# Kernel optimization log

Measured on AMD Instinct MI355X. Metric: run time of the kernel, lower is better.

Reference implementation:

```python
import jax, jax.numpy as jnp
import numpy as np

NS = 0.4      # neighborhood_size
GS = 8        # grid_size
RNN = 128     # rnn_size
EMB = 64      # embedding_size
NMIX = 20     # nmixtures
N = 1024      # num pedestrians


def setup_inputs() -> dict:
    key = jax.random.key(0)
    ks = jax.random.split(key, 14)
    s = 0.05
    return {
        "xoff": jax.random.normal(ks[0], (N, 2)) * s,
        "xabs": jax.random.uniform(ks[1], (N, 2)),
        "h0": jax.random.normal(ks[2], (1, N, RNN)) * 0.1,
        "c0": jax.random.normal(ks[3], (1, N, RNN)) * 0.1,
        "W_emb": jax.random.normal(ks[4], (EMB, 2)) * s,
        "b_emb": jax.random.normal(ks[5], (EMB,)) * s,
        "W_soc": jax.random.normal(ks[6], (EMB, GS * GS * RNN)) * s,
        "b_soc": jax.random.normal(ks[7], (EMB,)) * s,
        "W_ih": jax.random.normal(ks[8], (4 * RNN, 2 * EMB)) * s,
        "W_hh": jax.random.normal(ks[9], (4 * RNN, RNN)) * s,
        "b_ih": jax.random.normal(ks[10], (4 * RNN,)) * s,
        "b_hh": jax.random.normal(ks[11], (4 * RNN,)) * s,
        "W_out": jax.random.normal(ks[12], (6 * NMIX, RNN)) * s,
        "b_out": jax.random.normal(ks[13], (6 * NMIX,)) * s,
    }


def grid_mask(xabs, dtype):
    # Vectorized getGridMask: [N, N, GS*GS] one-hot neighbor binning.
    x, y = xabs[:, 0], xabs[:, 1]
    dx = x[None, :] - (x[:, None] - NS / 2)  # other_x - width_low, [N, N]
    dy = y[None, :] - (y[:, None] - NS / 2)
    cx = jnp.floor(dx / NS * GS).astype(jnp.int32)
    cy = jnp.floor(dy / NS * GS).astype(jnp.int32)
    n = x.shape[0]
    valid = ((dx >= 0) & (dx < NS) & (dy >= 0) & (dy < NS)
             & (cx >= 0) & (cx < GS) & (cy >= 0) & (cy < GS)
             & ~jnp.eye(n, dtype=bool))
    cell = jnp.clip(cx + cy * GS, 0, GS * GS - 1)
    return jax.nn.one_hot(cell, GS * GS, dtype=dtype) * valid[..., None].astype(dtype)


def reference(xoff, xabs, h0, c0, W_emb, b_emb, W_soc, b_soc,
              W_ih, W_hh, b_ih, b_hh, W_out, b_out):
    n = xabs.shape[0]
    # predict_distance=True -> embed offsets
    emb = jax.nn.relu(xoff @ W_emb.T + b_emb)                 # [N, 64]
    grid = grid_mask(xabs, emb.dtype)                          # [N, N, 64]
    h = h0[0]                                                  # [N, 128]
    # getSocialTensor: scatter neighbor hidden states into grid bins
    social = jnp.einsum('nmg,mh->ngh', grid, h).reshape(n, GS * GS * RNN)
    pool = jax.nn.relu(social @ W_soc.T + b_soc)               # [N, 64]
    xin = jnp.concatenate([emb, pool], axis=-1)                # [N, 128]
    # single-step LSTM, torch gate order i, f, g, o
    gates = xin @ W_ih.T + h @ W_hh.T + b_ih + b_hh            # [N, 512]
    i, f, g, o = jnp.split(gates, 4, axis=-1)
    c = jax.nn.sigmoid(f) * c0[0] + jax.nn.sigmoid(i) * jnp.tanh(g)
    hn = jax.nn.sigmoid(o) * jnp.tanh(c)
    out = hn @ W_out.T + b_out                                 # [N, 120]
    mu1, mu2, ls1, ls2, rho, pi_logits = jnp.split(out, 6, axis=1)
    return (mu1, mu2, ls1, ls2, rho, pi_logits)
```

## Files before the change

### kernel.cpp

```cpp
#include <hip/hip_runtime.h>
#include <hip/hip_bf16.h>

#define NN_ 1024

#define U_WGF  0
#define U_SHI  131072
#define U_ACTH 655360
#define U_P    917504
#define F_WOUT 2555904
#define F_HN   2572288
#define I_OFF  2703360
#define I_CNT  3751936

typedef __attribute__((ext_vector_type(8))) short short8;
typedef __attribute__((ext_vector_type(4))) float floatx4;

__device__ __forceinline__ float b2f_(unsigned short u) {
    return __uint_as_float(((unsigned)u) << 16);
}
__device__ __forceinline__ unsigned short f2bu(float f) {
    __hip_bfloat16 b = __float2bfloat16(f);
    return *(unsigned short*)&b;
}
__device__ __forceinline__ float ldin(const void* p, int i, int isbf) {
    return isbf ? b2f_(((const unsigned short*)p)[i]) : ((const float*)p)[i];
}
__device__ __forceinline__ int detect_bf16(const void* Wih, int tid) {
    unsigned wv = ((const unsigned*)Wih)[tid];
    unsigned e8 = (wv >> 7) & 0xFFu;
    return (__syncthreads_count((e8 >= 96u && e8 <= 134u) ? 1 : 0) > 128) ? 1 : 0;
}

__global__ __launch_bounds__(256) void prep_kernel(
        const void* __restrict__ xoff, const void* __restrict__ xabs,
        const void* __restrict__ h0,
        const void* __restrict__ Wsoc, const void* __restrict__ Wemb,
        const void* __restrict__ bemb, const void* __restrict__ Wih,
        const void* __restrict__ Whh,  const void* __restrict__ Wout,
        float* __restrict__ ws) {
    const int tid = threadIdx.x;
    const int bid = blockIdx.x;
    const int isbf = detect_bf16(Wih, tid);
    unsigned short* u = (unsigned short*)ws;

    if (bid < 424) {
        const int t0 = (bid * 256 + tid) * 8;
        unsigned short hv[8];
        if (t0 < 131072) {
            int jl = (t0 >> 3) & 15, q = (t0 >> 7) & 3, kb = (t0 >> 9) & 7, jt = t0 >> 12;
            int j = (jt & 3) * 128 + (jt >> 2) * 16 + jl;
            int k0 = kb * 32 + q * 8;
#pragma unroll
            for (int r = 0; r < 8; r++) {
                int k = k0 + r;
                float v = (k < 128) ? ldin(Wih, j * 128 + k, isbf)
                                    : ldin(Whh, j * 128 + (k - 128), isbf);
                hv[r] = f2bu(v);
            }
            *(short8*)(u + U_WGF + t0) = *(short8*)hv;
        } else if (t0 < 147456) {
            int t2 = t0 - 131072; int r = t2 >> 7, j0 = t2 & 127;
#pragma unroll
            for (int i = 0; i < 8; i++) {
                int j = j0 + i;
                ws[F_WOUT + t2 + i] = (j < 120) ? ldin(Wout, j * 128 + r, isbf) : 0.0f;
            }
        } else if (t0 < 671744) {
            int t2 = t0 - 147456;
            int e = (t2 >> 3) & 63, q = (t2 >> 9) & 3, j = (t2 >> 11) & 3, g = t2 >> 13;
            int src = e * 8192 + g * 128 + j * 32 + q * 8;
#pragma unroll
            for (int r = 0; r < 8; r++) hv[r] = f2bu(ldin(Wsoc, src + r, isbf));
            *(short8*)(u + U_SHI + t2) = *(short8*)hv;
        } else if (t0 < 802816) {
            int t2 = t0 - 671744; int n = t2 >> 7, k = t2 & 127;
#pragma unroll
            for (int i = 0; i < 8; i++) hv[i] = f2bu(ldin(h0, t2 + i, isbf));
            *(short8*)(u + U_ACTH + n * 256 + 128 + k) = *(short8*)hv;
        } else {
            int t2 = t0 - 802816; int n = t2 >> 6, e0 = t2 & 63;
            float x0 = ldin(xoff, 2 * n, isbf), x1 = ldin(xoff, 2 * n + 1, isbf);
#pragma unroll
            for (int i = 0; i < 8; i++) {
                int e = e0 + i;
                float v = fmaf(x0, ldin(Wemb, 2 * e, isbf),
                          fmaf(x1, ldin(Wemb, 2 * e + 1, isbf), ldin(bemb, e, isbf)));
                hv[i] = f2bu(fmaxf(v, 0.0f));
            }
            *(short8*)(u + U_ACTH + n * 256 + e0) = *(short8*)hv;
        }
    } else {
        __shared__ float xs_[2048];
        __shared__ int cnt_s[4];
        for (int i = tid; i < 2048; i += 256) xs_[i] = ldin(xabs, i, isbf);
        if (tid < 4) cnt_s[tid] = 0;
        __syncthreads();
        const int a = tid >> 6, t = tid & 63;
        const int n = (bid - 424) * 4 + a;
        unsigned* OFF = (unsigned*)ws + I_OFF + n * 1024;
        const float xsn = xs_[2 * n]     - 0.2f;
        const float ysn = xs_[2 * n + 1] - 0.2f;
        for (int i = t; i < NN_; i += 64) {
            float dx = xs_[2 * i]     - xsn;
            float dy = xs_[2 * i + 1] - ysn;
            int cx = (int)floorf(dx / 0.4f * 8.0f);
            int cy = (int)floorf(dy / 0.4f * 8.0f);
            bool valid = (dx >= 0.0f) && (dx < 0.4f) && (dy >= 0.0f) && (dy < 0.4f)
                      && (cx >= 0) && (cx < 8) && (cy >= 0) && (cy < 8) && (i != n);
            if (valid) {
                int pos = atomicAdd(&cnt_s[a], 1);
                OFF[pos] = (unsigned)(i * 4096 + ((cy * 8 + cx) << 6));
            }
        }
        __syncthreads();
        if (tid < 4) ((unsigned*)ws)[I_CNT + (bid - 424) * 4 + tid] = (unsigned)cnt_s[tid];
    }
}

__global__ __launch_bounds__(256) void pgemm_kernel(float* __restrict__ ws) {
    const unsigned short* u = (const unsigned short*)ws;
    const short* Ah  = (const short*)(u + U_ACTH);
    const short* Shi = (const short*)(u + U_SHI);
    unsigned short* P16 = (unsigned short*)ws + U_P;
    const int tid = threadIdx.x, lane = tid & 63, wv = tid >> 6;
    const int B_ = blockIdx.y * 64 + blockIdx.x;
    const int mtile = B_ & 63, rest = B_ >> 6;
    const int cg = rest >> 1, thalf = rest & 1;
    const int m = lane & 15, q = lane >> 4;
    const int g = cg * 4 + wv;
    const int abase = (mtile * 16 + m) * 256 + 128 + q * 8;
    short8 ah[4];
#pragma unroll
    for (int j = 0; j < 4; j++) ah[j] = *(const short8*)(Ah + abase + 32 * j);
    const int rowl = mtile * 16 + q * 4;
#pragma unroll
    for (int tt = 0; tt < 2; tt++) {
        const int t = thalf * 2 + tt;
        const int e = t * 16 + m;
        floatx4 c = {0.0f, 0.0f, 0.0f, 0.0f};
#pragma unroll
        for (int j = 0; j < 4; j++) {
            short8 bh = *(const short8*)(Shi + ((g * 4 + j) * 4 + q) * 512 + e * 8);
            c = __builtin_amdgcn_mfma_f32_16x16x32_bf16(ah[j], bh, c, 0, 0, 0);
        }
        const int n0 = cg * 256 + wv * 64 + t * 16;
#pragma unroll
        for (int r = 0; r < 4; r++)
            P16[(rowl + r) * 4096 + n0 + m] = f2bu(c[r]);
    }
}

__global__ __launch_bounds__(256) void pool_kernel(const void* __restrict__ b_soc,
                                                   const void* __restrict__ Wih_det,
                                                   float* __restrict__ ws) {
    __shared__ int off_s[1024];
    __shared__ float4 red4[16][16];
    const int tid = threadIdx.x;
    const int isbf = detect_bf16(Wih_det, tid);
    const int n = blockIdx.x;
    unsigned short* u = (unsigned short*)ws;
    const int cc = (int)((const unsigned*)ws)[I_CNT + n];
    {
        const unsigned* lst = (const unsigned*)ws + I_OFF + n * 1024;
        for (int j = tid; j < cc; j += 256) off_s[j] = (int)lst[j];
    }
    __syncthreads();
    {
        const unsigned short* P16 = (const unsigned short*)ws + U_P;
        const int strm = tid >> 4, e4 = tid & 15;
        float ax = 0.0f, ay = 0.0f, az = 0.0f, aw = 0.0f;
        for (int j = strm; j < cc; j += 16) {
            int o = off_s[j];
            ushort4 uu = *(const ushort4*)(P16 + o + 4 * e4);
            ax += b2f_(uu.x); ay += b2f_(uu.y); az += b2f_(uu.z); aw += b2f_(uu.w);
        }
        red4[strm][e4] = make_float4(ax, ay, az, aw);
    }
    __syncthreads();
    if (tid < 16) {
        float s[4] = {0.0f, 0.0f, 0.0f, 0.0f};
#pragma unroll
        for (int s16 = 0; s16 < 16; s16++) {
            float4 r = red4[s16][tid];
            s[0] += r.x; s[1] += r.y; s[2] += r.z; s[3] += r.w;
        }
        int e = 4 * tid;
#pragma unroll
        for (int i = 0; i < 4; i++) {
            float v = fmaxf(s[i] + ldin(b_soc, e + i, isbf), 0.0f);
            u[U_ACTH + n * 256 + 64 + e + i] = f2bu(v);
        }
    }
}

__global__ __launch_bounds__(256) void gates_kernel(const void* __restrict__ c0,
                                                    const void* __restrict__ b_ih,
                                                    const void* __restrict__ b_hh,
                                                    const void* __restrict__ Wih_det,
                                                    float* __restrict__ ws) {
    __shared__ float gl[16][68];
    const int tid = threadIdx.x;
    const int isbf = detect_bf16(Wih_det, tid);
    const unsigned short* u = (const unsigned short*)ws;
    const short* Ah = (const short*)(u + U_ACTH);
    const short* Wg = (const short*)(u + U_WGF);
    const int lane = tid & 63, wv = tid >> 6, m = lane & 15, q = lane >> 4;
    const int m0 = blockIdx.x * 16, y = blockIdx.y;
    const int jt = y * 4 + wv;
    floatx4 acc = {0.0f, 0.0f, 0.0f, 0.0f};
#pragma unroll
    for (int kb = 0; kb < 8; kb++) {
        short8 ah = *(const short8*)(Ah + (m0 + m) * 256 + kb * 32 + q * 8);
        short8 b  = *(const short8*)(Wg + (jt * 8 + kb) * 512 + q * 128 + m * 8);
        acc = __builtin_amdgcn_mfma_f32_16x16x32_bf16(ah, b, acc, 0, 0, 0);
    }
    const int jorig = wv * 128 + y * 16 + m;
    const float bias = ldin(b_ih, jorig, isbf) + ldin(b_hh, jorig, isbf);
#pragma unroll
    for (int r = 0; r < 4; r++)
        gl[q * 4 + r][wv * 16 + m] = acc[r] + bias;
    __syncthreads();
    {
        const int a = tid >> 4, rl = tid & 15;
        const int n = m0 + a, rg = y * 16 + rl;
        float iv = gl[a][rl],      fv = gl[a][16 + rl];
        float gv = gl[a][32 + rl], ov = gl[a][48 + rl];
        float si = 1.0f / (1.0f + expf(-iv));
        float sf = 1.0f / (1.0f + expf(-fv));
        float so = 1.0f / (1.0f + expf(-ov));
        float cc = sf * ldin(c0, n * 128 + rg, isbf) + si * tanhf(gv);
        ws[F_HN + n * 128 + rg] = so * tanhf(cc);
    }
}

__global__ __launch_bounds__(256) void pwout_kernel(const void* __restrict__ b_out,
                                                    const void* __restrict__ Wih_det,
                                                    const float* __restrict__ ws,
                                                    float* __restrict__ out) {
    __shared__ __align__(16) float hnl[2][128];
    const int tid = threadIdx.x;
    const int isbf = detect_bf16(Wih_det, tid);
    const int n0 = blockIdx.x * 2;
    const int half = tid >> 7, t2 = tid & 127;
    const int n = n0 + half;
    hnl[half][t2] = ws[F_HN + n * 128 + t2];
    __syncthreads();
    if (t2 < 120) {
        int j = t2;
        float acc = ldin(b_out, j, isbf);
        for (int r = 0; r < 128; r += 4) {
            float4 hq = *(const float4*)&hnl[half][r];
            acc = fmaf(hq.x, ws[F_WOUT + (r + 0) * 128 + j], acc);
            acc = fmaf(hq.y, ws[F_WOUT + (r + 1) * 128 + j], acc);
            acc = fmaf(hq.z, ws[F_WOUT + (r + 2) * 128 + j], acc);
            acc = fmaf(hq.w, ws[F_WOUT + (r + 3) * 128 + j], acc);
        }
        int ch = j / 20, wc = j - ch * 20;
        out[ch * 20480 + n * 20 + wc] = acc;
    }
}

extern "C" void kernel_launch(void* const* d_in, const int* in_sizes, int n_in,
                              void* d_out, int out_size, void* d_ws, size_t ws_size,
                              hipStream_t stream) {
    const void* xoff  = d_in[0];
    const void* xabs  = d_in[1];
    const void* h0    = d_in[2];
    const void* c0    = d_in[3];
    const void* W_emb = d_in[4];
    const void* b_emb = d_in[5];
    const void* W_soc = d_in[6];
    const void* b_soc = d_in[7];
    const void* W_ih  = d_in[8];
    const void* W_hh  = d_in[9];
    const void* b_ih  = d_in[10];
    const void* b_hh  = d_in[11];
    const void* W_out = d_in[12];
    const void* b_out = d_in[13];
    float* ws = (float*)d_ws;
    float* out = (float*)d_out;

    prep_kernel<<<680, 256, 0, stream>>>(xoff, xabs, h0, W_soc, W_emb, b_emb,
                                         W_ih, W_hh, W_out, ws);
    pgemm_kernel<<<dim3(64, 32), 256, 0, stream>>>(ws);
    pool_kernel<<<1024, 256, 0, stream>>>(b_soc, W_ih, ws);
    gates_kernel<<<dim3(64, 8), 256, 0, stream>>>(c0, b_ih, b_hh, W_ih, ws);
    pwout_kernel<<<512, 256, 0, stream>>>(b_out, W_ih, ws, out);
}
```

Before: 117.2 us.

## Redistribute prep work across kernels and widen pool gather loads

Moves neighbor-list binning from the prep kernel into the pgemm launch, and moves the gate-weight, W_out and embedding preparation into the pool launch as extra blocks. The prep kernel shrinks to W_soc and h0 conversion, so less work sits on the critical path before the projection GEMM and independent work runs alongside dependent work. The pool gather now uses 16-byte loads, 32 streams and a 4-way unrolled loop for more memory-level parallelism. In exchange, heterogeneous blocks share a launch and the shared-memory footprint of the pool kernel grows.

New measurement: 118.4 us. Within noise of the previous version (+1.0%).

```diff
diff --git a/kernel.cpp b/kernel.cpp
--- a/kernel.cpp
+++ b/kernel.cpp
@@ -32,62 +32,64 @@
 }
 
 __global__ __launch_bounds__(256) void prep_kernel(
-        const void* __restrict__ xoff, const void* __restrict__ xabs,
-        const void* __restrict__ h0,
-        const void* __restrict__ Wsoc, const void* __restrict__ Wemb,
-        const void* __restrict__ bemb, const void* __restrict__ Wih,
-        const void* __restrict__ Whh,  const void* __restrict__ Wout,
-        float* __restrict__ ws) {
-    const int tid = threadIdx.x;
-    const int bid = blockIdx.x;
+        const void* __restrict__ h0,  const void* __restrict__ Wsoc,
+        const void* __restrict__ Wih, float* __restrict__ ws) {
+    const int tid = threadIdx.x;
     const int isbf = detect_bf16(Wih, tid);
     unsigned short* u = (unsigned short*)ws;
-
-    if (bid < 424) {
-        const int t0 = (bid * 256 + tid) * 8;
-        unsigned short hv[8];
-        if (t0 < 131072) {
-            int jl = (t0 >> 3) & 15, q = (t0 >> 7) & 3, kb = (t0 >> 9) & 7, jt = t0 >> 12;
-            int j = (jt & 3) * 128 + (jt >> 2) * 16 + jl;
-            int k0 = kb * 32 + q * 8;
-#pragma unroll
-            for (int r = 0; r < 8; r++) {
-                int k = k0 + r;
-                float v = (k < 128) ? ldin(Wih, j * 128 + k, isbf)
-                                    : ldin(Whh, j * 128 + (k - 128), isbf);
-                hv[r] = f2bu(v);
+    const int t0 = 147456 + (blockIdx.x * 256 + tid) * 8;
+    unsigned short hv[8];
+    if (t0 < 671744) {
+        int t2 = t0 - 147456;
+        int e = (t2 >> 3) & 63, q = (t2 >> 9) & 3, j = (t2 >> 11) & 3, g = t2 >> 13;
+        int src = e * 8192 + g * 128 + j * 32 + q * 8;
+#pragma unroll
+        for (int r = 0; r < 8; r++) hv[r] = f2bu(ldin(Wsoc, src + r, isbf));
+        *(short8*)(u + U_SHI + t2) = *(short8*)hv;
+    } else {
+        int t2 = t0 - 671744; int n = t2 >> 7, k = t2 & 127;
+#pragma unroll
+        for (int i = 0; i < 8; i++) hv[i] = f2bu(ldin(h0, t2 + i, isbf));
+        *(short8*)(u + U_ACTH + n * 256 + 128 + k) = *(short8*)hv;
+    }
+}
+
+__global__ __launch_bounds__(256) void pgemm_kernel(const void* __restrict__ xabs,
+                                                    const void* __restrict__ Wih_det,
+                                                    float* __restrict__ ws) {
+    const int tid = threadIdx.x;
+    const int bid = blockIdx.x;
+    const int isbf = detect_bf16(Wih_det, tid);
+    const unsigned short* u = (const unsigned short*)ws;
+
+    if (bid < 2048) {
+        const short* Ah  = (const short*)(u + U_ACTH);
+        const short* Shi = (const short*)(u + U_SHI);
+        unsigned short* P16 = (unsigned short*)ws + U_P;
+        const int lane = tid & 63, wv = tid >> 6;
+        const int mtile = bid & 63, rest = bid >> 6;
+        const int cg = rest >> 1, thalf = rest & 1;
+        const int m = lane & 15, q = lane >> 4;
+        const int g = cg * 4 + wv;
+        const int abase = (mtile * 16 + m) * 256 + 128 + q * 8;
+        short8 ah[4];
+#pragma unroll
+        for (int j = 0; j < 4; j++) ah[j] = *(const short8*)(Ah + abase + 32 * j);
+        const int rowl = mtile * 16 + q * 4;
+#pragma unroll
+        for (int tt = 0; tt < 2; tt++) {
+            const int t = thalf * 2 + tt;
+            const int e = t * 16 + m;
+            floatx4 c = {0.0f, 0.0f, 0.0f, 0.0f};
+#pragma unroll
+            for (int j = 0; j < 4; j++) {
+                short8 bh = *(const short8*)(Shi + ((g * 4 + j) * 4 + q) * 512 + e * 8);
+                c = __builtin_amdgcn_mfma_f32_16x16x32_bf16(ah[j], bh, c, 0, 0, 0);
             }
-            *(short8*)(u + U_WGF + t0) = *(short8*)hv;
-        } else if (t0 < 147456) {
-            int t2 = t0 - 131072; int r = t2 >> 7, j0 = t2 & 127;
-#pragma unroll
-            for (int i = 0; i < 8; i++) {
-                int j = j0 + i;
-                ws[F_WOUT + t2 + i] = (j < 120) ? ldin(Wout, j * 128 + r, isbf) : 0.0f;
-            }
-        } else if (t0 < 671744) {
-            int t2 = t0 - 147456;
-            int e = (t2 >> 3) & 63, q = (t2 >> 9) & 3, j = (t2 >> 11) & 3, g = t2 >> 13;
-            int src = e * 8192 + g * 128 + j * 32 + q * 8;
-#pragma unroll
-            for (int r = 0; r < 8; r++) hv[r] = f2bu(ldin(Wsoc, src + r, isbf));
-            *(short8*)(u + U_SHI + t2) = *(short8*)hv;
-        } else if (t0 < 802816) {
-            int t2 = t0 - 671744; int n = t2 >> 7, k = t2 & 127;
-#pragma unroll
-            for (int i = 0; i < 8; i++) hv[i] = f2bu(ldin(h0, t2 + i, isbf));
-            *(short8*)(u + U_ACTH + n * 256 + 128 + k) = *(short8*)hv;
-        } else {
-            int t2 = t0 - 802816; int n = t2 >> 6, e0 = t2 & 63;
-            float x0 = ldin(xoff, 2 * n, isbf), x1 = ldin(xoff, 2 * n + 1, isbf);
-#pragma unroll
-            for (int i = 0; i < 8; i++) {
-                int e = e0 + i;
-                float v = fmaf(x0, ldin(Wemb, 2 * e, isbf),
-                          fmaf(x1, ldin(Wemb, 2 * e + 1, isbf), ldin(bemb, e, isbf)));
-                hv[i] = f2bu(fmaxf(v, 0.0f));
-            }
-            *(short8*)(u + U_ACTH + n * 256 + e0) = *(short8*)hv;
+            const int n0 = cg * 256 + wv * 64 + t * 16;
+#pragma unroll
+            for (int r = 0; r < 4; r++)
+                P16[(rowl + r) * 4096 + n0 + m] = f2bu(c[r]);
         }
     } else {
         __shared__ float xs_[2048];
@@ -96,7 +98,7 @@
         if (tid < 4) cnt_s[tid] = 0;
         __syncthreads();
         const int a = tid >> 6, t = tid & 63;
-        const int n = (bid - 424) * 4 + a;
+        const int n = (bid - 2048) * 4 + a;
         unsigned* OFF = (unsigned*)ws + I_OFF + n * 1024;
         const float xsn = xs_[2 * n]     - 0.2f;
         const float ysn = xs_[2 * n + 1] - 0.2f;
@@ -113,83 +115,100 @@
             }
         }
         __syncthreads();
-        if (tid < 4) ((unsigned*)ws)[I_CNT + (bid - 424) * 4 + tid] = (unsigned)cnt_s[tid];
-    }
-}
-
-__global__ __launch_bounds__(256) void pgemm_kernel(float* __restrict__ ws) {
-    const unsigned short* u = (const unsigned short*)ws;
-    const short* Ah  = (const short*)(u + U_ACTH);
-    const short* Shi = (const short*)(u + U_SHI);
-    unsigned short* P16 = (unsigned short*)ws + U_P;
-    const int tid = threadIdx.x, lane = tid & 63, wv = tid >> 6;
-    const int B_ = blockIdx.y * 64 + blockIdx.x;
-    const int mtile = B_ & 63, rest = B_ >> 6;
-    const int cg = rest >> 1, thalf = rest & 1;
-    const int m = lane & 15, q = lane >> 4;
-    const int g = cg * 4 + wv;
-    const int abase = (mtile * 16 + m) * 256 + 128 + q * 8;
-    short8 ah[4];
-#pragma unroll
-    for (int j = 0; j < 4; j++) ah[j] = *(const short8*)(Ah + abase + 32 * j);
-    const int rowl = mtile * 16 + q * 4;
-#pragma unroll
-    for (int tt = 0; tt < 2; tt++) {
-        const int t = thalf * 2 + tt;
-        const int e = t * 16 + m;
-        floatx4 c = {0.0f, 0.0f, 0.0f, 0.0f};
-#pragma unroll
-        for (int j = 0; j < 4; j++) {
-            short8 bh = *(const short8*)(Shi + ((g * 4 + j) * 4 + q) * 512 + e * 8);
-            c = __builtin_amdgcn_mfma_f32_16x16x32_bf16(ah[j], bh, c, 0, 0, 0);
-        }
-        const int n0 = cg * 256 + wv * 64 + t * 16;
-#pragma unroll
-        for (int r = 0; r < 4; r++)
-            P16[(rowl + r) * 4096 + n0 + m] = f2bu(c[r]);
-    }
-}
-
-__global__ __launch_bounds__(256) void pool_kernel(const void* __restrict__ b_soc,
-                                                   const void* __restrict__ Wih_det,
-                                                   float* __restrict__ ws) {
+        if (tid < 4) ((unsigned*)ws)[I_CNT + (bid - 2048) * 4 + tid] = (unsigned)cnt_s[tid];
+    }
+}
+
+__global__ __launch_bounds__(256) void pool_kernel(
+        const void* __restrict__ xoff, const void* __restrict__ Wemb,
+        const void* __restrict__ bemb, const void* __restrict__ b_soc,
+        const void* __restrict__ Wih,  const void* __restrict__ Whh,
+        const void* __restrict__ Wout, float* __restrict__ ws) {
     __shared__ int off_s[1024];
-    __shared__ float4 red4[16][16];
-    const int tid = threadIdx.x;
-    const int isbf = detect_bf16(Wih_det, tid);
-    const int n = blockIdx.x;
+    __shared__ float red[32][64];
+    const int tid = threadIdx.x;
+    const int isbf = detect_bf16(Wih, tid);
+    const int bid = blockIdx.x;
     unsigned short* u = (unsigned short*)ws;
-    const int cc = (int)((const unsigned*)ws)[I_CNT + n];
-    {
-        const unsigned* lst = (const unsigned*)ws + I_OFF + n * 1024;
-        for (int j = tid; j < cc; j += 256) off_s[j] = (int)lst[j];
-    }
-    __syncthreads();
-    {
-        const unsigned short* P16 = (const unsigned short*)ws + U_P;
-        const int strm = tid >> 4, e4 = tid & 15;
-        float ax = 0.0f, ay = 0.0f, az = 0.0f, aw = 0.0f;
-        for (int j = strm; j < cc; j += 16) {
-            int o = off_s[j];
-            ushort4 uu = *(const ushort4*)(P16 + o + 4 * e4);
-            ax += b2f_(uu.x); ay += b2f_(uu.y); az += b2f_(uu.z); aw += b2f_(uu.w);
-        }
-        red4[strm][e4] = make_float4(ax, ay, az, aw);
-    }
-    __syncthreads();
-    if (tid < 16) {
-        float s[4] = {0.0f, 0.0f, 0.0f, 0.0f};
-#pragma unroll
-        for (int s16 = 0; s16 < 16; s16++) {
-            float4 r = red4[s16][tid];
-            s[0] += r.x; s[1] += r.y; s[2] += r.z; s[3] += r.w;
-        }
-        int e = 4 * tid;
-#pragma unroll
-        for (int i = 0; i < 4; i++) {
-            float v = fmaxf(s[i] + ldin(b_soc, e + i, isbf), 0.0f);
-            u[U_ACTH + n * 256 + 64 + e + i] = f2bu(v);
-        }
+
+    if (bid < 1024) {
+        const int n = bid;
+        const int cc = (int)((const unsigned*)ws)[I_CNT + n];
+        {
+            const unsigned* lst = (const unsigned*)ws + I_OFF + n * 1024;
+            for (int j = tid; j < cc; j += 256) off_s[j] = (int)lst[j];
+        }
+        __syncthreads();
+        {
+            const unsigned short* P16 = (const unsigned short*)ws + U_P;
+            const int strm = tid >> 3, l = tid & 7;
+            float acc[8] = {0.f, 0.f, 0.f, 0.f, 0.f, 0.f, 0.f, 0.f};
+            int j = strm;
+            while (j + 96 < cc) {
+                int o0 = off_s[j], o1 = off_s[j + 32], o2 = off_s[j + 64], o3 = off_s[j + 96];
+                short8 v0 = *(const short8*)(P16 + o0 + l * 8);
+                short8 v1 = *(const short8*)(P16 + o1 + l * 8);
+                short8 v2 = *(const short8*)(P16 + o2 + l * 8);
+                short8 v3 = *(const short8*)(P16 + o3 + l * 8);
+#pragma unroll
+                for (int i = 0; i < 8; i++)
+                    acc[i] += b2f_((unsigned short)v0[i]) + b2f_((unsigned short)v1[i])
+                            + b2f_((unsigned short)v2[i]) + b2f_((unsigned short)v3[i]);
+                j += 128;
+            }
+            while (j < cc) {
+                int o0 = off_s[j];
+                short8 v0 = *(const short8*)(P16 + o0 + l * 8);
+#pragma unroll
+                for (int i = 0; i < 8; i++) acc[i] += b2f_((unsigned short)v0[i]);
+                j += 32;
+            }
+#pragma unroll
+            for (int i = 0; i < 8; i++) red[strm][l * 8 + i] = acc[i];
+        }
+        __syncthreads();
+        if (tid < 64) {
+            float s = 0.0f;
+#pragma unroll
+            for (int s32 = 0; s32 < 32; s32++) s += red[s32][tid];
+            float v = fmaxf(s + ldin(b_soc, tid, isbf), 0.0f);
+            u[U_ACTH + n * 256 + 64 + tid] = f2bu(v);
+        }
+    } else if (bid < 1088) {
+        const int t0 = (bid - 1024) * 2048 + tid * 8;
+        const int jl = (t0 >> 3) & 15, q = (t0 >> 7) & 3, kb = (t0 >> 9) & 7, jt = t0 >> 12;
+        const int j = (jt & 3) * 128 + (jt >> 2) * 16 + jl;
+        const int k0 = kb * 32 + q * 8;
+        unsigned short hv[8];
+#pragma unroll
+        for (int r = 0; r < 8; r++) {
+            int k = k0 + r;
+            float v = (k < 128) ? ldin(Wih, j * 128 + k, isbf)
+                                : ldin(Whh, j * 128 + (k - 128), isbf);
+            hv[r] = f2bu(v);
+        }
+        *(short8*)(u + U_WGF + t0) = *(short8*)hv;
+    } else if (bid < 1096) {
+        const int t2 = (bid - 1088) * 2048 + tid * 8;
+        const int r = t2 >> 7, j0 = t2 & 127;
+#pragma unroll
+        for (int i = 0; i < 8; i++) {
+            int j = j0 + i;
+            ws[F_WOUT + t2 + i] = (j < 120) ? ldin(Wout, j * 128 + r, isbf) : 0.0f;
+        }
+    } else {
+        const int t2 = (bid - 1096) * 2048 + tid * 8;
+        const int n = t2 >> 6, e0 = t2 & 63;
+        const float x0 = ldin(xoff, 2 * n, isbf), x1 = ldin(xoff, 2 * n + 1, isbf);
+        unsigned short hv[8];
+#pragma unroll
+        for (int i = 0; i < 8; i++) {
+            int e = e0 + i;
+            float v = fmaf(x0, ldin(Wemb, 2 * e, isbf),
+                      fmaf(x1, ldin(Wemb, 2 * e + 1, isbf), ldin(bemb, e, isbf)));
+            hv[i] = f2bu(fmaxf(v, 0.0f));
+        }
+        *(short8*)(u + U_ACTH + n * 256 + e0) = *(short8*)hv;
     }
 }
 
@@ -280,10 +299,10 @@
     float* ws = (float*)d_ws;
     float* out = (float*)d_out;
 
-    prep_kernel<<<680, 256, 0, stream>>>(xoff, xabs, h0, W_soc, W_emb, b_emb,
-                                         W_ih, W_hh, W_out, ws);
-    pgemm_kernel<<<dim3(64, 32), 256, 0, stream>>>(ws);
-    pool_kernel<<<1024, 256, 0, stream>>>(b_soc, W_ih, ws);
+    prep_kernel<<<320, 256, 0, stream>>>(h0, W_soc, W_ih, ws);
+    pgemm_kernel<<<2304, 256, 0, stream>>>(xabs, W_ih, ws);
+    pool_kernel<<<1128, 256, 0, stream>>>(xoff, W_emb, b_emb, b_soc,
+                                          W_ih, W_hh, W_out, ws);
     gates_kernel<<<dim3(64, 8), 256, 0, stream>>>(c0, b_ih, b_hh, W_ih, ws);
     pwout_kernel<<<512, 256, 0, stream>>>(b_out, W_ih, ws, out);
 }
```

## Fuse five kernel launches into one cooperative mega-kernel with grid syncs

Applied to the files above, without the earlier changes.

Merges the prep, pgemm, pool, gates and output-projection stages into a single cooperative kernel of 1024 blocks, separated by grid.sync() barriers, with shared memory reused across stages. This removes four kernel launch gaps and their inter-kernel drain. The cost is grid-wide barriers, forcing all 1024 blocks to be co-resident (launch bounds set to 4 blocks per CU), and some stages leaving half the blocks idle. It falls back to the old multi-kernel path if cooperative launch is unavailable or occupancy is too low.

New measurement: 118.3 us. Within noise of the previous version (+0.9%).

```diff
diff --git a/kernel.cpp b/kernel.cpp
--- a/kernel.cpp
+++ b/kernel.cpp
@@ -1,5 +1,8 @@
 #include <hip/hip_runtime.h>
+#include <hip/hip_cooperative_groups.h>
 #include <hip/hip_bf16.h>
+
+namespace cg = cooperative_groups;
 
 #define NN_ 1024
 
@@ -31,17 +34,21 @@
     return (__syncthreads_count((e8 >= 96u && e8 <= 134u) ? 1 : 0) > 128) ? 1 : 0;
 }
 
-__global__ __launch_bounds__(256) void prep_kernel(
+__global__ __launch_bounds__(256, 4) void mega_kernel(
         const void* __restrict__ xoff, const void* __restrict__ xabs,
-        const void* __restrict__ h0,
-        const void* __restrict__ Wsoc, const void* __restrict__ Wemb,
-        const void* __restrict__ bemb, const void* __restrict__ Wih,
-        const void* __restrict__ Whh,  const void* __restrict__ Wout,
-        float* __restrict__ ws) {
+        const void* __restrict__ h0,   const void* __restrict__ c0,
+        const void* __restrict__ Wemb, const void* __restrict__ bemb,
+        const void* __restrict__ Wsoc, const void* __restrict__ bsoc,
+        const void* __restrict__ Wih,  const void* __restrict__ Whh,
+        const void* __restrict__ bih,  const void* __restrict__ bhh,
+        const void* __restrict__ Wout, const void* __restrict__ bout,
+        float* __restrict__ ws,        float* __restrict__ out) {
     const int tid = threadIdx.x;
     const int bid = blockIdx.x;
     const int isbf = detect_bf16(Wih, tid);
     unsigned short* u = (unsigned short*)ws;
+    __shared__ __align__(16) char smem[8704];
+    cg::grid_group grid = cg::this_grid();
 
     if (bid < 424) {
         const int t0 = (bid * 256 + tid) * 8;
@@ -89,9 +96,9 @@
             }
             *(short8*)(u + U_ACTH + n * 256 + e0) = *(short8*)hv;
         }
-    } else {
-        __shared__ float xs_[2048];
-        __shared__ int cnt_s[4];
+    } else if (bid < 680) {
+        float* xs_  = (float*)smem;
+        int*  cnt_s = (int*)(smem + 8192);
         for (int i = tid; i < 2048; i += 256) xs_[i] = ldin(xabs, i, isbf);
         if (tid < 4) cnt_s[tid] = 0;
         __syncthreads();
@@ -115,6 +122,224 @@
         __syncthreads();
         if (tid < 4) ((unsigned*)ws)[I_CNT + (bid - 424) * 4 + tid] = (unsigned)cnt_s[tid];
     }
+    grid.sync();
+
+    {
+        const short* Ah  = (const short*)(u + U_ACTH);
+        const short* Shi = (const short*)(u + U_SHI);
+        unsigned short* P16 = u + U_P;
+        const int lane = tid & 63, wv = tid >> 6;
+        const int m = lane & 15, q = lane >> 4;
+#pragma unroll
+        for (int u2 = 0; u2 < 2; ++u2) {
+            const int B_ = bid * 2 + u2;
+            const int mtile = B_ & 63, rest = B_ >> 6;
+            const int cgn = rest >> 1, thalf = rest & 1;
+            const int g = cgn * 4 + wv;
+            const int abase = (mtile * 16 + m) * 256 + 128 + q * 8;
+            short8 ah[4];
+#pragma unroll
+            for (int j = 0; j < 4; j++) ah[j] = *(const short8*)(Ah + abase + 32 * j);
+            const int rowl = mtile * 16 + q * 4;
+#pragma unroll
+            for (int tt = 0; tt < 2; tt++) {
+                const int t = thalf * 2 + tt;
+                const int e = t * 16 + m;
+                floatx4 c = {0.0f, 0.0f, 0.0f, 0.0f};
+#pragma unroll
+                for (int j = 0; j < 4; j++) {
+                    short8 bh = *(const short8*)(Shi + ((g * 4 + j) * 4 + q) * 512 + e * 8);
+                    c = __builtin_amdgcn_mfma_f32_16x16x32_bf16(ah[j], bh, c, 0, 0, 0);
+                }
+                const int n0 = cgn * 256 + wv * 64 + t * 16;
+#pragma unroll
+                for (int r = 0; r < 4; r++)
+                    P16[(rowl + r) * 4096 + n0 + m] = f2bu(c[r]);
+            }
+        }
+    }
+    grid.sync();
+
+    {
+        int*    off_s = (int*)smem;
+        float4 (*red4)[16] = (float4(*)[16])(smem + 4096);
+        const int n = bid;
+        const int cc = (int)((const unsigned*)ws)[I_CNT + n];
+        {
+            const unsigned* lst = (const unsigned*)ws + I_OFF + n * 1024;
+            for (int j = tid; j < cc; j += 256) off_s[j] = (int)lst[j];
+        }
+        __syncthreads();
+        {
+            const unsigned short* P16 = (const unsigned short*)ws + U_P;
+            const int strm = tid >> 4, e4 = tid & 15;
+            float ax = 0.0f, ay = 0.0f, az = 0.0f, aw = 0.0f;
+            for (int j = strm; j < cc; j += 16) {
+                int o = off_s[j];
+                ushort4 uu = *(const ushort4*)(P16 + o + 4 * e4);
+                ax += b2f_(uu.x); ay += b2f_(uu.y); az += b2f_(uu.z); aw += b2f_(uu.w);
+            }
+            red4[strm][e4] = make_float4(ax, ay, az, aw);
+        }
+        __syncthreads();
+        if (tid < 16) {
+            float s[4] = {0.0f, 0.0f, 0.0f, 0.0f};
+#pragma unroll
+            for (int s16 = 0; s16 < 16; s16++) {
+                float4 r = red4[s16][tid];
+                s[0] += r.x; s[1] += r.y; s[2] += r.z; s[3] += r.w;
+            }
+            int e = 4 * tid;
+#pragma unroll
+            for (int i = 0; i < 4; i++) {
+                float v = fmaxf(s[i] + ldin(bsoc, e + i, isbf), 0.0f);
+                u[U_ACTH + n * 256 + 64 + e + i] = f2bu(v);
+            }
+        }
+    }
+    grid.sync();
+
+    if (bid < 512) {
+        float (*gl)[68] = (float(*)[68])smem;
+        const short* Ah = (const short*)(u + U_ACTH);
+        const short* Wg = (const short*)(u + U_WGF);
+        const int lane = tid & 63, wv = tid >> 6, m = lane & 15, q = lane >> 4;
+        const int m0 = (bid & 63) * 16, y = bid >> 6;
+        const int jt = y * 4 + wv;
+        floatx4 acc = {0.0f, 0.0f, 0.0f, 0.0f};
+#pragma unroll
+        for (int kb = 0; kb < 8; kb++) {
+            short8 ah = *(const short8*)(Ah + (m0 + m) * 256 + kb * 32 + q * 8);
+            short8 b  = *(const short8*)(Wg + (jt * 8 + kb) * 512 + q * 128 + m * 8);
+            acc = __builtin_amdgcn_mfma_f32_16x16x32_bf16(ah, b, acc, 0, 0, 0);
+        }
+        const int jorig = wv * 128 + y * 16 + m;
+        const float bias = ldin(bih, jorig, isbf) + ldin(bhh, jorig, isbf);
+#pragma unroll
+        for (int r = 0; r < 4; r++)
+            gl[q * 4 + r][wv * 16 + m] = acc[r] + bias;
+        __syncthreads();
+        {
+            const int a = tid >> 4, rl = tid & 15;
+            const int n = m0 + a, rg = y * 16 + rl;
+            float iv = gl[a][rl],      fv = gl[a][16 + rl];
+            float gv = gl[a][32 + rl], ov = gl[a][48 + rl];
+            float si = 1.0f / (1.0f + expf(-iv));
+            float sf = 1.0f / (1.0f + expf(-fv));
+            float so = 1.0f / (1.0f + expf(-ov));
+            float cc = sf * ldin(c0, n * 128 + rg, isbf) + si * tanhf(gv);
+            ws[F_HN + n * 128 + rg] = so * tanhf(cc);
+        }
+    }
+    grid.sync();
+
+    if (bid < 512) {
+        float (*hnl)[128] = (float(*)[128])smem;
+        const int n0 = bid * 2;
+        const int half = tid >> 7, t2 = tid & 127;
+        const int n = n0 + half;
+        hnl[half][t2] = ws[F_HN + n * 128 + t2];
+        __syncthreads();
+        if (t2 < 120) {
+            int j = t2;
+            float acc = ldin(bout, j, isbf);
+            for (int r = 0; r < 128; r += 4) {
+                float4 hq = *(const float4*)&hnl[half][r];
+                acc = fmaf(hq.x, ws[F_WOUT + (r + 0) * 128 + j], acc);
+                acc = fmaf(hq.y, ws[F_WOUT + (r + 1) * 128 + j], acc);
+                acc = fmaf(hq.z, ws[F_WOUT + (r + 2) * 128 + j], acc);
+                acc = fmaf(hq.w, ws[F_WOUT + (r + 3) * 128 + j], acc);
+            }
+            int ch = j / 20, wc = j - ch * 20;
+            out[ch * 20480 + n * 20 + wc] = acc;
+        }
+    }
+}
+
+__global__ __launch_bounds__(256) void prep_kernel(
+        const void* __restrict__ xoff, const void* __restrict__ xabs,
+        const void* __restrict__ h0,
+        const void* __restrict__ Wsoc, const void* __restrict__ Wemb,
+        const void* __restrict__ bemb, const void* __restrict__ Wih,
+        const void* __restrict__ Whh,  const void* __restrict__ Wout,
+        float* __restrict__ ws) {
+    const int tid = threadIdx.x;
+    const int bid = blockIdx.x;
+    const int isbf = detect_bf16(Wih, tid);
+    unsigned short* u = (unsigned short*)ws;
+
+    if (bid < 424) {
+        const int t0 = (bid * 256 + tid) * 8;
+        unsigned short hv[8];
+        if (t0 < 131072) {
+            int jl = (t0 >> 3) & 15, q = (t0 >> 7) & 3, kb = (t0 >> 9) & 7, jt = t0 >> 12;
+            int j = (jt & 3) * 128 + (jt >> 2) * 16 + jl;
+            int k0 = kb * 32 + q * 8;
+#pragma unroll
+            for (int r = 0; r < 8; r++) {
+                int k = k0 + r;
+                float v = (k < 128) ? ldin(Wih, j * 128 + k, isbf)
+                                    : ldin(Whh, j * 128 + (k - 128), isbf);
+                hv[r] = f2bu(v);
+            }
+            *(short8*)(u + U_WGF + t0) = *(short8*)hv;
+        } else if (t0 < 147456) {
+            int t2 = t0 - 131072; int r = t2 >> 7, j0 = t2 & 127;
+#pragma unroll
+            for (int i = 0; i < 8; i++) {
+                int j = j0 + i;
+                ws[F_WOUT + t2 + i] = (j < 120) ? ldin(Wout, j * 128 + r, isbf) : 0.0f;
+            }
+        } else if (t0 < 671744) {
+            int t2 = t0 - 147456;
+            int e = (t2 >> 3) & 63, q = (t2 >> 9) & 3, j = (t2 >> 11) & 3, g = t2 >> 13;
+            int src = e * 8192 + g * 128 + j * 32 + q * 8;
+#pragma unroll
+            for (int r = 0; r < 8; r++) hv[r] = f2bu(ldin(Wsoc, src + r, isbf));
+            *(short8*)(u + U_SHI + t2) = *(short8*)hv;
+        } else if (t0 < 802816) {
+            int t2 = t0 - 671744; int n = t2 >> 7, k = t2 & 127;
+#pragma unroll
+            for (int i = 0; i < 8; i++) hv[i] = f2bu(ldin(h0, t2 + i, isbf));
+            *(short8*)(u + U_ACTH + n * 256 + 128 + k) = *(short8*)hv;
+        } else {
+            int t2 = t0 - 802816; int n = t2 >> 6, e0 = t2 & 63;
+            float x0 = ldin(xoff, 2 * n, isbf), x1 = ldin(xoff, 2 * n + 1, isbf);
+#pragma unroll
+            for (int i = 0; i < 8; i++) {
+                int e = e0 + i;
+                float v = fmaf(x0, ldin(Wemb, 2 * e, isbf),
+                          fmaf(x1, ldin(Wemb, 2 * e + 1, isbf), ldin(bemb, e, isbf)));
+                hv[i] = f2bu(fmaxf(v, 0.0f));
+            }
+            *(short8*)(u + U_ACTH + n * 256 + e0) = *(short8*)hv;
+        }
+    } else {
+        __shared__ float xs_[2048];
+        __shared__ int cnt_s[4];
+        for (int i = tid; i < 2048; i += 256) xs_[i] = ldin(xabs, i, isbf);
+        if (tid < 4) cnt_s[tid] = 0;
+        __syncthreads();
+        const int a = tid >> 6, t = tid & 63;
+        const int n = (bid - 424) * 4 + a;
+        unsigned* OFF = (unsigned*)ws + I_OFF + n * 1024;
+        const float xsn = xs_[2 * n]     - 0.2f;
+        const float ysn = xs_[2 * n + 1] - 0.2f;
+        for (int i = t; i < NN_; i += 64) {
+            float dx = xs_[2 * i]     - xsn;
+            float dy = xs_[2 * i + 1] - ysn;
+            int cx = (int)floorf(dx / 0.4f * 8.0f);
+            int cy = (int)floorf(dy / 0.4f * 8.0f);
+            bool valid = (dx >= 0.0f) && (dx < 0.4f) && (dy >= 0.0f) && (dy < 0.4f)
+                      && (cx >= 0) && (cx < 8) && (cy >= 0) && (cy < 8) && (i != n);
+            if (valid) {
+                int pos = atomicAdd(&cnt_s[a], 1);
+                OFF[pos] = (unsigned)(i * 4096 + ((cy * 8 + cx) << 6));
+            }
+        }
+        __syncthreads();
+        if (tid < 4) ((unsigned*)ws)[I_CNT + (bid - 424) * 4 + tid] = (unsigned)cnt_s[tid];
+    }
 }
 
 __global__ __launch_bounds__(256) void pgemm_kernel(float* __restrict__ ws) {
@@ -125,9 +350,9 @@
     const int tid = threadIdx.x, lane = tid & 63, wv = tid >> 6;
     const int B_ = blockIdx.y * 64 + blockIdx.x;
     const int mtile = B_ & 63, rest = B_ >> 6;
-    const int cg = rest >> 1, thalf = rest & 1;
+    const int cgn = rest >> 1, thalf = rest & 1;
     const int m = lane & 15, q = lane >> 4;
-    const int g = cg * 4 + wv;
+    const int g = cgn * 4 + wv;
     const int abase = (mtile * 16 + m) * 256 + 128 + q * 8;
     short8 ah[4];
 #pragma unroll
@@ -143,7 +368,7 @@
             short8 bh = *(const short8*)(Shi + ((g * 4 + j) * 4 + q) * 512 + e * 8);
             c = __builtin_amdgcn_mfma_f32_16x16x32_bf16(ah[j], bh, c, 0, 0, 0);
         }
-        const int n0 = cg * 256 + wv * 64 + t * 16;
+        const int n0 = cgn * 256 + wv * 64 + t * 16;
 #pragma unroll
         for (int r = 0; r < 4; r++)
             P16[(rowl + r) * 4096 + n0 + m] = f2bu(c[r]);
@@ -280,6 +505,30 @@
     float* ws = (float*)d_ws;
     float* out = (float*)d_out;
 
+    static int use_coop = -1;
+    if (use_coop < 0) {
+        int nb = 0, ncu = 0, dev = 0, coop = 0;
+        hipError_t e1 = hipOccupancyMaxActiveBlocksPerMultiprocessor(
+                            &nb, (const void*)mega_kernel, 256, 0);
+        hipGetDevice(&dev);
+        hipError_t e2 = hipDeviceGetAttribute(&ncu, hipDeviceAttributeMultiprocessorCount, dev);
+        hipError_t e3 = hipDeviceGetAttribute(&coop, hipDeviceAttributeCooperativeLaunch, dev);
+        use_coop = (e1 == hipSuccess && e2 == hipSuccess && e3 == hipSuccess &&
+                    coop != 0 && nb * ncu >= 1024) ? 1 : 0;
+    }
+
+    if (use_coop) {
+        void* args[] = {(void*)&xoff, (void*)&xabs, (void*)&h0, (void*)&c0,
+                        (void*)&W_emb, (void*)&b_emb, (void*)&W_soc, (void*)&b_soc,
+                        (void*)&W_ih, (void*)&W_hh, (void*)&b_ih, (void*)&b_hh,
+                        (void*)&W_out, (void*)&b_out, (void*)&ws, (void*)&out};
+        hipError_t e = hipLaunchCooperativeKernel((const void*)mega_kernel,
+                                                  dim3(1024), dim3(256),
+                                                  args, 0, stream);
+        if (e == hipSuccess) return;
+        use_coop = 0;
+    }
+
     prep_kernel<<<680, 256, 0, stream>>>(xoff, xabs, h0, W_soc, W_emb, b_emb,
                                          W_ih, W_hh, W_out, ws);
     pgemm_kernel<<<dim3(64, 32), 256, 0, stream>>>(ws);
```

## Fuse prep with h0·Wsoc GEMM and fold output projection into gates kernel

Applied to the files above, without the earlier changes.

Removes the separate pgemm kernel. h0 and W_soc are now read and converted to bf16 directly inside the first kernel's MFMA tiles, with no repacked staging copy. The output projection also moves into the gates kernel: each y-block adds its 16-row partial product into a zeroed output with float atomics. This cuts two launches and the workspace round-trips, at the cost of a memset, atomic contention across 8 y-blocks, and strided W_soc reads that are no longer prepacked.

Result: no change. 118.0 us (+0.6%).

```diff
diff --git a/kernel.cpp b/kernel.cpp
--- a/kernel.cpp
+++ b/kernel.cpp
@@ -4,11 +4,9 @@
 #define NN_ 1024
 
 #define U_WGF  0
-#define U_SHI  131072
 #define U_ACTH 655360
 #define U_P    917504
 #define F_WOUT 2555904
-#define F_HN   2572288
 #define I_OFF  2703360
 #define I_CNT  3751936
 
@@ -30,73 +28,71 @@
     unsigned e8 = (wv >> 7) & 0xFFu;
     return (__syncthreads_count((e8 >= 96u && e8 <= 134u) ? 1 : 0) > 128) ? 1 : 0;
 }
-
-__global__ __launch_bounds__(256) void prep_kernel(
+__device__ __forceinline__ short8 ld8_bf(const void* p, int idx, int isbf) {
+    if (isbf) return *(const short8*)((const unsigned short*)p + idx);
+    const float4* f = (const float4*)((const float*)p + idx);
+    float4 a = f[0], b = f[1];
+    short8 r;
+    r[0] = (short)f2bu(a.x); r[1] = (short)f2bu(a.y);
+    r[2] = (short)f2bu(a.z); r[3] = (short)f2bu(a.w);
+    r[4] = (short)f2bu(b.x); r[5] = (short)f2bu(b.y);
+    r[6] = (short)f2bu(b.z); r[7] = (short)f2bu(b.w);
+    return r;
+}
+
+__global__ __launch_bounds__(256) void fused1_kernel(
         const void* __restrict__ xoff, const void* __restrict__ xabs,
-        const void* __restrict__ h0,
-        const void* __restrict__ Wsoc, const void* __restrict__ Wemb,
-        const void* __restrict__ bemb, const void* __restrict__ Wih,
-        const void* __restrict__ Whh,  const void* __restrict__ Wout,
-        float* __restrict__ ws) {
+        const void* __restrict__ h0,   const void* __restrict__ Wsoc,
+        const void* __restrict__ Wemb, const void* __restrict__ bemb,
+        const void* __restrict__ Wih,  const void* __restrict__ Whh,
+        const void* __restrict__ Wout, float* __restrict__ ws) {
     const int tid = threadIdx.x;
     const int bid = blockIdx.x;
     const int isbf = detect_bf16(Wih, tid);
     unsigned short* u = (unsigned short*)ws;
 
-    if (bid < 424) {
-        const int t0 = (bid * 256 + tid) * 8;
-        unsigned short hv[8];
-        if (t0 < 131072) {
-            int jl = (t0 >> 3) & 15, q = (t0 >> 7) & 3, kb = (t0 >> 9) & 7, jt = t0 >> 12;
-            int j = (jt & 3) * 128 + (jt >> 2) * 16 + jl;
-            int k0 = kb * 32 + q * 8;
-#pragma unroll
-            for (int r = 0; r < 8; r++) {
-                int k = k0 + r;
-                float v = (k < 128) ? ldin(Wih, j * 128 + k, isbf)
-                                    : ldin(Whh, j * 128 + (k - 128), isbf);
-                hv[r] = f2bu(v);
+    if (bid < 512) {
+        unsigned short* P16 = u + U_P;
+        const int mg = bid >> 4, ng = bid & 15;
+        const int lane = tid & 63, wv = tid >> 6;
+        const int m = lane & 15, q = lane >> 4;
+        short8 ah[2][4];
+#pragma unroll
+        for (int mt = 0; mt < 2; ++mt) {
+            const int row = mg * 32 + mt * 16 + m;
+#pragma unroll
+            for (int kb = 0; kb < 4; ++kb)
+                ah[mt][kb] = ld8_bf(h0, row * 128 + kb * 32 + q * 8, isbf);
+        }
+#pragma unroll
+        for (int c = 0; c < 4; ++c) {
+            const int ct = wv * 4 + c;
+            const int col = ng * 256 + ct * 16 + m;
+            const int g = col >> 6, e = col & 63;
+            short8 bf[4];
+#pragma unroll
+            for (int kb = 0; kb < 4; ++kb)
+                bf[kb] = ld8_bf(Wsoc, e * 8192 + g * 128 + kb * 32 + q * 8, isbf);
+            floatx4 c0_ = {0.f, 0.f, 0.f, 0.f}, c1_ = {0.f, 0.f, 0.f, 0.f};
+#pragma unroll
+            for (int kb = 0; kb < 4; ++kb) {
+                c0_ = __builtin_amdgcn_mfma_f32_16x16x32_bf16(ah[0][kb], bf[kb], c0_, 0, 0, 0);
+                c1_ = __builtin_amdgcn_mfma_f32_16x16x32_bf16(ah[1][kb], bf[kb], c1_, 0, 0, 0);
             }
-            *(short8*)(u + U_WGF + t0) = *(short8*)hv;
-        } else if (t0 < 147456) {
-            int t2 = t0 - 131072; int r = t2 >> 7, j0 = t2 & 127;
-#pragma unroll
-            for (int i = 0; i < 8; i++) {
-                int j = j0 + i;
-                ws[F_WOUT + t2 + i] = (j < 120) ? ldin(Wout, j * 128 + r, isbf) : 0.0f;
+#pragma unroll
+            for (int r = 0; r < 4; ++r) {
+                P16[(mg * 32 + q * 4 + r) * 4096 + col]      = f2bu(c0_[r]);
+                P16[(mg * 32 + 16 + q * 4 + r) * 4096 + col] = f2bu(c1_[r]);
             }
-        } else if (t0 < 671744) {
-            int t2 = t0 - 147456;
-            int e = (t2 >> 3) & 63, q = (t2 >> 9) & 3, j = (t2 >> 11) & 3, g = t2 >> 13;
-            int src = e * 8192 + g * 128 + j * 32 + q * 8;
-#pragma unroll
-            for (int r = 0; r < 8; r++) hv[r] = f2bu(ldin(Wsoc, src + r, isbf));
-            *(short8*)(u + U_SHI + t2) = *(short8*)hv;
-        } else if (t0 < 802816) {
-            int t2 = t0 - 671744; int n = t2 >> 7, k = t2 & 127;
-#pragma unroll
-            for (int i = 0; i < 8; i++) hv[i] = f2bu(ldin(h0, t2 + i, isbf));
-            *(short8*)(u + U_ACTH + n * 256 + 128 + k) = *(short8*)hv;
-        } else {
-            int t2 = t0 - 802816; int n = t2 >> 6, e0 = t2 & 63;
-            float x0 = ldin(xoff, 2 * n, isbf), x1 = ldin(xoff, 2 * n + 1, isbf);
-#pragma unroll
-            for (int i = 0; i < 8; i++) {
-                int e = e0 + i;
-                float v = fmaf(x0, ldin(Wemb, 2 * e, isbf),
-                          fmaf(x1, ldin(Wemb, 2 * e + 1, isbf), ldin(bemb, e, isbf)));
-                hv[i] = f2bu(fmaxf(v, 0.0f));
-            }
-            *(short8*)(u + U_ACTH + n * 256 + e0) = *(short8*)hv;
-        }
-    } else {
+        }
+    } else if (bid < 768) {
         __shared__ float xs_[2048];
         __shared__ int cnt_s[4];
         for (int i = tid; i < 2048; i += 256) xs_[i] = ldin(xabs, i, isbf);
         if (tid < 4) cnt_s[tid] = 0;
         __syncthreads();
         const int a = tid >> 6, t = tid & 63;
-        const int n = (bid - 424) * 4 + a;
+        const int n = (bid - 512) * 4 + a;
         unsigned* OFF = (unsigned*)ws + I_OFF + n * 1024;
         const float xsn = xs_[2 * n]     - 0.2f;
         const float ysn = xs_[2 * n + 1] - 0.2f;
@@ -113,40 +109,49 @@
             }
         }
         __syncthreads();
-        if (tid < 4) ((unsigned*)ws)[I_CNT + (bid - 424) * 4 + tid] = (unsigned)cnt_s[tid];
-    }
-}
-
-__global__ __launch_bounds__(256) void pgemm_kernel(float* __restrict__ ws) {
-    const unsigned short* u = (const unsigned short*)ws;
-    const short* Ah  = (const short*)(u + U_ACTH);
-    const short* Shi = (const short*)(u + U_SHI);
-    unsigned short* P16 = (unsigned short*)ws + U_P;
-    const int tid = threadIdx.x, lane = tid & 63, wv = tid >> 6;
-    const int B_ = blockIdx.y * 64 + blockIdx.x;
-    const int mtile = B_ & 63, rest = B_ >> 6;
-    const int cg = rest >> 1, thalf = rest & 1;
-    const int m = lane & 15, q = lane >> 4;
-    const int g = cg * 4 + wv;
-    const int abase = (mtile * 16 + m) * 256 + 128 + q * 8;
-    short8 ah[4];
-#pragma unroll
-    for (int j = 0; j < 4; j++) ah[j] = *(const short8*)(Ah + abase + 32 * j);
-    const int rowl = mtile * 16 + q * 4;
-#pragma unroll
-    for (int tt = 0; tt < 2; tt++) {
-        const int t = thalf * 2 + tt;
-        const int e = t * 16 + m;
-        floatx4 c = {0.0f, 0.0f, 0.0f, 0.0f};
-#pragma unroll
-        for (int j = 0; j < 4; j++) {
-            short8 bh = *(const short8*)(Shi + ((g * 4 + j) * 4 + q) * 512 + e * 8);
-            c = __builtin_amdgcn_mfma_f32_16x16x32_bf16(ah[j], bh, c, 0, 0, 0);
-        }
-        const int n0 = cg * 256 + wv * 64 + t * 16;
-#pragma unroll
-        for (int r = 0; r < 4; r++)
-            P16[(rowl + r) * 4096 + n0 + m] = f2bu(c[r]);
+        if (tid < 4) ((unsigned*)ws)[I_CNT + (bid - 512) * 4 + tid] = (unsigned)cnt_s[tid];
+    } else if (bid < 832) {
+        const int t0 = (bid - 768) * 2048 + tid * 8;
+        const int jl = (t0 >> 3) & 15, q = (t0 >> 7) & 3, kb = (t0 >> 9) & 7, jt = t0 >> 12;
+        const int j = (jt & 3) * 128 + (jt >> 2) * 16 + jl;
+        const int k0 = kb * 32 + q * 8;
+        unsigned short hv[8];
+#pragma unroll
+        for (int r = 0; r < 8; r++) {
+            int k = k0 + r;
+            float v = (k < 128) ? ldin(Wih, j * 128 + k, isbf)
+                                : ldin(Whh, j * 128 + (k - 128), isbf);
+            hv[r] = f2bu(v);
+        }
+        *(short8*)(u + U_WGF + t0) = *(short8*)hv;
+    } else if (bid < 840) {
+        const int t2 = (bid - 832) * 2048 + tid * 8;
+        const int r = t2 >> 7, j0 = t2 & 127;
+#pragma unroll
+        for (int i = 0; i < 8; i++) {
+            int j = j0 + i;
+            ws[F_WOUT + t2 + i] = (j < 120) ? ldin(Wout, j * 128 + r, isbf) : 0.0f;
+        }
+    } else if (bid < 872) {
+        const int t2 = (bid - 840) * 2048 + tid * 8;
+        const int n = t2 >> 6, e0 = t2 & 63;
+        const float x0 = ldin(xoff, 2 * n, isbf), x1 = ldin(xoff, 2 * n + 1, isbf);
+        unsigned short hv[8];
+#pragma unroll
+        for (int i = 0; i < 8; i++) {
+            int e = e0 + i;
+            float v = fmaf(x0, ldin(Wemb, 2 * e, isbf),
+                      fmaf(x1, ldin(Wemb, 2 * e + 1, isbf), ldin(bemb, e, isbf)));
+            hv[i] = f2bu(fmaxf(v, 0.0f));
+        }
+        *(short8*)(u + U_ACTH + n * 256 + e0) = *(short8*)hv;
+    } else {
+        const int t2 = (bid - 872) * 2048 + tid * 8;
+        const int n = t2 >> 7, k = t2 & 127;
+        unsigned short hv[8];
+#pragma unroll
+        for (int i = 0; i < 8; i++) hv[i] = f2bu(ldin(h0, t2 + i, isbf));
+        *(short8*)(u + U_ACTH + n * 256 + 128 + k) = *(short8*)hv;
     }
 }
 
@@ -196,9 +201,12 @@
 __global__ __launch_bounds__(256) void gates_kernel(const void* __restrict__ c0,
                                                     const void* __restrict__ b_ih,
                                                     const void* __restrict__ b_hh,
+                                                    const void* __restrict__ b_out,
                                                     const void* __restrict__ Wih_det,
-                                                    float* __restrict__ ws) {
+                                                    const float* __restrict__ ws,
+                                                    float* __restrict__ out) {
     __shared__ float gl[16][68];
+    __shared__ float hnl[16][16];
     const int tid = threadIdx.x;
     const int isbf = detect_bf16(Wih_det, tid);
     const unsigned short* u = (const unsigned short*)ws;
@@ -229,34 +237,21 @@
         float sf = 1.0f / (1.0f + expf(-fv));
         float so = 1.0f / (1.0f + expf(-ov));
         float cc = sf * ldin(c0, n * 128 + rg, isbf) + si * tanhf(gv);
-        ws[F_HN + n * 128 + rg] = so * tanhf(cc);
-    }
-}
-
-__global__ __launch_bounds__(256) void pwout_kernel(const void* __restrict__ b_out,
-                                                    const void* __restrict__ Wih_det,
-                                                    const float* __restrict__ ws,
-                                                    float* __restrict__ out) {
-    __shared__ __align__(16) float hnl[2][128];
-    const int tid = threadIdx.x;
-    const int isbf = detect_bf16(Wih_det, tid);
-    const int n0 = blockIdx.x * 2;
-    const int half = tid >> 7, t2 = tid & 127;
-    const int n = n0 + half;
-    hnl[half][t2] = ws[F_HN + n * 128 + t2];
-    __syncthreads();
-    if (t2 < 120) {
-        int j = t2;
-        float acc = ldin(b_out, j, isbf);
-        for (int r = 0; r < 128; r += 4) {
-            float4 hq = *(const float4*)&hnl[half][r];
-            acc = fmaf(hq.x, ws[F_WOUT + (r + 0) * 128 + j], acc);
-            acc = fmaf(hq.y, ws[F_WOUT + (r + 1) * 128 + j], acc);
-            acc = fmaf(hq.z, ws[F_WOUT + (r + 2) * 128 + j], acc);
-            acc = fmaf(hq.w, ws[F_WOUT + (r + 3) * 128 + j], acc);
-        }
-        int ch = j / 20, wc = j - ch * 20;
-        out[ch * 20480 + n * 20 + wc] = acc;
+        hnl[a][rl] = so * tanhf(cc);
+    }
+    __syncthreads();
+    {
+        const int a = tid >> 4, jb = tid & 15;
+        const int n = m0 + a;
+        const float* WT = ws + F_WOUT + (y * 16) * 128;
+        for (int j = jb; j < 120; j += 16) {
+            float acc2 = (y == 0) ? ldin(b_out, j, isbf) : 0.0f;
+#pragma unroll
+            for (int rl = 0; rl < 16; ++rl)
+                acc2 = fmaf(hnl[a][rl], WT[rl * 128 + j], acc2);
+            int ch = j / 20, wc = j - ch * 20;
+            atomicAdd(&out[ch * 20480 + n * 20 + wc], acc2);
+        }
     }
 }
 
@@ -280,10 +275,10 @@
     float* ws = (float*)d_ws;
     float* out = (float*)d_out;
 
-    prep_kernel<<<680, 256, 0, stream>>>(xoff, xabs, h0, W_soc, W_emb, b_emb,
-                                         W_ih, W_hh, W_out, ws);
-    pgemm_kernel<<<dim3(64, 32), 256, 0, stream>>>(ws);
+    hipMemsetAsync(d_out, 0, (size_t)out_size, stream);
+    fused1_kernel<<<936, 256, 0, stream>>>(xoff, xabs, h0, W_soc, W_emb, b_emb,
+                                           W_ih, W_hh, W_out, ws);
     pool_kernel<<<1024, 256, 0, stream>>>(b_soc, W_ih, ws);
-    gates_kernel<<<dim3(64, 8), 256, 0, stream>>>(c0, b_ih, b_hh, W_ih, ws);
-    pwout_kernel<<<512, 256, 0, stream>>>(b_out, W_ih, ws, out);
-}
+    gates_kernel<<<dim3(64, 8), 256, 0, stream>>>(c0, b_ih, b_hh, b_out,
+                                                  W_ih, ws, out);
+}
```
